# Kernel optimization log

Hardware: AMD Instinct MI355X
Metric: run time of the kernel (lower is better)

## Reference

```python
import jax, jax.numpy as jnp
import numpy as np


def setup_inputs() -> dict:
    key = jax.random.key(0)
    ks = jax.random.split(key, 8)
    b, s1, s2 = 16, 512, 40
    video_dim, text_dim, attn_dim = 1024, 300, 256
    return {
        "video": jax.random.normal(ks[0], (b, s1, video_dim), dtype=jnp.float32),
        "text": jax.random.normal(ks[1], (b, s2, text_dim), dtype=jnp.float32),
        "w1": jax.random.normal(ks[2], (video_dim, attn_dim), dtype=jnp.float32),
        "w2": jax.random.normal(ks[3], (text_dim, attn_dim), dtype=jnp.float32),
        "w3": jax.random.normal(ks[4], (attn_dim, 1), dtype=jnp.float32),
        "bias": jax.random.normal(ks[5], (attn_dim,), dtype=jnp.float32),
        "w4": jax.random.normal(ks[6], (4 * attn_dim, 500), dtype=jnp.float32),
        "b4": jax.random.normal(ks[7], (500,), dtype=jnp.float32),
    }


def reference(video, text, w1, w2, w3, bias, w4, b4):
    # video: (b, s1, d1), text: (b, s2, d2)
    e = jnp.einsum("bsd,da->bsa", video, w1)   # (b, s1, a) -- also 'hh' in original
    f = jnp.einsum("btd,da->bta", text, w2)    # (b, s2, a)
    # additive attention energies: tanh over (b, s1, s2, a) broadcast sum
    h = jnp.tanh(e[:, :, None, :] + f[:, None, :, :] + bias)  # (b, s1, s2, a)
    logits = jnp.squeeze(jnp.einsum("bsta,ao->bsto", h, w3), -1)  # (b, s1, s2)
    # original expands logits over attn_dim then softmaxes dim=2; identical to
    # softmax over s2 of the scalar scores, broadcast afterwards.
    attn = jax.nn.softmax(logits, axis=2)  # (b, s1, s2)
    text_attn = jnp.einsum("bst,bta->bsa", attn, f)  # (b, s1, a)
    cont = jnp.concatenate(
        [e, text_attn, e * text_attn, e - text_attn], axis=-1
    )  # (b, s1, 4a)
    return jnp.tanh(cont) @ w4 + b4  # (b, s1, 500)
```

## Files before the change

kernel.cpp:

```cpp
#include <hip/hip_runtime.h>
#include <hip/hip_bf16.h>
#include <cstdint>

typedef __attribute__((ext_vector_type(8))) short bf16x8;
typedef __attribute__((ext_vector_type(4))) short bf16x4;
typedef __attribute__((ext_vector_type(4))) float f32x4;

#define TANH_SCALE 2.8853900817779268f
#define TANH_UNSCALE 0.34657359027997264f

__device__ __forceinline__ short cvt_bf16(float f) {
  union { float f; uint32_t u; } x; x.f = f;
  uint32_t r = x.u + 0x7FFFu + ((x.u >> 16) & 1u);
  return (short)(r >> 16);
}
__device__ __forceinline__ float bf16_to_f(short s) {
  union { uint32_t u; float f; } x; x.u = ((uint32_t)(uint16_t)s) << 16;
  return x.f;
}

__device__ __forceinline__ float tanh_fast(float x) {
  float e = __builtin_amdgcn_exp2f(x * TANH_SCALE);
  return 1.0f - 2.0f * __builtin_amdgcn_rcpf(e + 1.0f);
}
__device__ __forceinline__ float sig_pre(float xs) {
  float e = __builtin_amdgcn_exp2f(xs);
  return __builtin_amdgcn_rcpf(e + 1.0f);
}

__device__ __forceinline__ void split8(float4 a, float4 b, bf16x8& h, bf16x8& l) {
  float fa[8] = {a.x, a.y, a.z, a.w, b.x, b.y, b.z, b.w};
  uint32_t uh[8], ul[8];
  #pragma unroll
  for (int j = 0; j < 8; j++) {
    union { float f; uint32_t u; } x; x.f = fa[j];
    uh[j] = x.u;
    union { uint32_t u; float f; } t; t.u = x.u & 0xffff0000u;
    union { float f; uint32_t u; } y; y.f = fa[j] - t.f;
    ul[j] = y.u;
  }
  union { uint32_t w[4]; bf16x8 v; } H, L;
  #pragma unroll
  for (int j = 0; j < 4; j++) {
    H.w[j] = __builtin_amdgcn_perm(uh[2 * j + 1], uh[2 * j], 0x07060302u);
    L.w[j] = __builtin_amdgcn_perm(ul[2 * j + 1], ul[2 * j], 0x07060302u);
  }
  h = H.v; l = L.v;
}

__global__ __launch_bounds__(256) void k_prep(const float* __restrict__ text,
                                              const float* __restrict__ w1,
                                              const float* __restrict__ w2,
                                              const float* __restrict__ w4,
                                              short* __restrict__ w1h,
                                              short* __restrict__ w1l,
                                              short* __restrict__ w4T,
                                              short* __restrict__ th,
                                              short* __restrict__ tl,
                                              short* __restrict__ w2h,
                                              short* __restrict__ w2l) {
  __shared__ float tile[32][33];
  int bid = blockIdx.x;
  if (bid < 256) {
    int idx = bid;
    int r0 = (idx & 31) * 32, c0 = (idx >> 5) * 32;
    int j = threadIdx.x & 31, i0 = threadIdx.x >> 5;
    #pragma unroll
    for (int i = i0; i < 32; i += 8) tile[i][j] = w1[(size_t)(r0 + i) * 256 + c0 + j];
    __syncthreads();
    #pragma unroll
    for (int i = i0; i < 32; i += 8) {
      float v = tile[j][i];
      short h = cvt_bf16(v);
      w1h[(size_t)(c0 + i) * 1024 + r0 + j] = h;
      w1l[(size_t)(c0 + i) * 1024 + r0 + j] = cvt_bf16(v - bf16_to_f(h));
    }
  } else if (bid < 768) {
    int idx = bid - 256;
    int r0 = (idx & 31) * 32, c0 = (idx >> 5) * 32;
    int j = threadIdx.x & 31, i0 = threadIdx.x >> 5;
    #pragma unroll
    for (int i = i0; i < 32; i += 8) {
      int c = c0 + j;
      tile[i][j] = (c < 500) ? w4[(size_t)(r0 + i) * 500 + c] : 0.f;
    }
    __syncthreads();
    #pragma unroll
    for (int i = i0; i < 32; i += 8)
      w4T[(size_t)(c0 + i) * 1024 + r0 + j] = cvt_bf16(tile[j][i]);
  } else if (bid < 928) {
    int idx = bid - 768;
    int row = idx * 4 + (threadIdx.x >> 6);
    int cl = threadIdx.x & 63;
    const float* trow = text + (size_t)row * 300;
    short* hrow = th + (size_t)row * 320;
    short* lrow = tl + (size_t)row * 320;
    #pragma unroll
    for (int c0 = 0; c0 < 320; c0 += 64) {
      int c = c0 + cl;
      float v = (c < 300) ? trow[c] : 0.f;
      short h = cvt_bf16(v);
      hrow[c] = h;
      lrow[c] = cvt_bf16(v - bf16_to_f(h));
    }
  } else {
    int idx = bid - 928;
    int rt = idx % 10, ct = idx / 10;
    int r0 = rt * 32, c0 = ct * 32;
    int j = threadIdx.x & 31, i0 = threadIdx.x >> 5;
    #pragma unroll
    for (int i = i0; i < 32; i += 8) {
      int r = r0 + i;
      tile[i][j] = (r < 300) ? w2[(size_t)r * 256 + c0 + j] : 0.f;
    }
    __syncthreads();
    #pragma unroll
    for (int i = i0; i < 32; i += 8) {
      float v = tile[j][i];
      short h = cvt_bf16(v);
      w2h[(size_t)(c0 + i) * 320 + r0 + j] = h;
      w2l[(size_t)(c0 + i) * 320 + r0 + j] = cvt_bf16(v - bf16_to_f(h));
    }
  }
}

__device__ __forceinline__ void load_lds16(void* lds, const void* g) {
  __builtin_amdgcn_global_load_lds(
      (const __attribute__((address_space(1))) void*)g,
      (__attribute__((address_space(3))) void*)lds, 16, 0, 0);
}

__global__ __launch_bounds__(256) void k_gemm_big(const float* __restrict__ video,
                                                  const short* __restrict__ w1h,
                                                  const short* __restrict__ w1l,
                                                  const short* __restrict__ th,
                                                  const short* __restrict__ tl,
                                                  const short* __restrict__ w2h,
                                                  const short* __restrict__ w2l,
                                                  float* __restrict__ eparts,
                                                  float* __restrict__ fbuf) {
  __shared__ __align__(16) char smem[65536];
  int bid = blockIdx.x;
  int tid = threadIdx.x, lane = tid & 63, wave = tid >> 6;
  int mrow = lane & 15, quad = lane >> 4;

  if (bid < 512) {
    short (*Ash)[64] = (short (*)[64])(smem);
    short (*Asl)[64] = (short (*)[64])(smem + 16384);
    int m0 = (bid & 63) * 128, n0 = ((bid >> 6) & 3) * 64;
    int z = bid >> 8;
    int kz0 = z * 512;
    int wm = wave * 32;
    int lrow = lane >> 3;
    int lsegsw = ((lane & 7) ^ lrow) * 8;

    f32x4 acc[2][4];
    #pragma unroll
    for (int i = 0; i < 2; i++)
      #pragma unroll
      for (int j = 0; j < 4; j++) acc[i][j] = (f32x4){0.f, 0.f, 0.f, 0.f};

    auto stageB = [&](int k0, int buf) {
      short* Bh = (short*)(smem + 32768 + buf * 8192);
      short* Bl = (short*)(smem + 49152 + buf * 8192);
      #pragma unroll
      for (int i = 0; i < 2; i++) {
        int c = wave * 2 + i;
        size_t go = (size_t)(n0 + c * 8 + lrow) * 1024 + k0 + lsegsw;
        load_lds16(Bh + (size_t)(c * 8) * 64, w1h + go);
        load_lds16(Bl + (size_t)(c * 8) * 64, w1l + go);
      }
    };
    auto loadA = [&](int k0, float4* va) {
      #pragma unroll
      for (int it = 0; it < 4; it++) {
        int idx = it * 256 + tid;
        const float* src = video + (size_t)(m0 + (idx >> 3)) * 1024 + k0 + (idx & 7) * 8;
        va[it * 2]     = *(const float4*)src;
        va[it * 2 + 1] = *(const float4*)(src + 4);
      }
    };

    float4 va[8];
    stageB(kz0, 0);
    loadA(kz0, va);

    for (int t = 0; t < 8; t++) {
      int k0 = kz0 + t * 64;
      int cur = t & 1;
      bf16x8 hi[4], lo[4];
      #pragma unroll
      for (int it = 0; it < 4; it++) split8(va[it * 2], va[it * 2 + 1], hi[it], lo[it]);
      __builtin_amdgcn_s_barrier();
      #pragma unroll
      for (int it = 0; it < 4; it++) {
        int idx = it * 256 + tid;
        int row = idx >> 3;
        int sw = ((idx & 7) ^ (row & 7)) * 8;
        *(bf16x8*)&Ash[row][sw] = hi[it];
        *(bf16x8*)&Asl[row][sw] = lo[it];
      }
      if (t + 1 < 8) {
        stageB(k0 + 64, cur ^ 1);
        loadA(k0 + 64, va);
        asm volatile("s_waitcnt vmcnt(12)" ::: "memory");
      } else {
        asm volatile("s_waitcnt vmcnt(0)" ::: "memory");
      }
      asm volatile("s_waitcnt lgkmcnt(0)" ::: "memory");
      __builtin_amdgcn_s_barrier();
      const short* Bh = (const short*)(smem + 32768 + cur * 8192);
      const short* Bl = (const short*)(smem + 49152 + cur * 8192);
      int rsw = mrow & 7;
      #pragma unroll
      for (int ks = 0; ks < 2; ks++) {
        int slot = ks * 4 + quad;
        int kko = ((slot ^ rsw) & 7) * 8;
        bf16x8 ah[2], al[2], bh[4], bl[4];
        #pragma unroll
        for (int i = 0; i < 2; i++) {
          ah[i] = *(const bf16x8*)&Ash[wm + i * 16 + mrow][kko];
          al[i] = *(const bf16x8*)&Asl[wm + i * 16 + mrow][kko];
        }
        #pragma unroll
        for (int j = 0; j < 4; j++) {
          bh[j] = *(const bf16x8*)&Bh[(size_t)(j * 16 + mrow) * 64 + kko];
          bl[j] = *(const bf16x8*)&Bl[(size_t)(j * 16 + mrow) * 64 + kko];
        }
        #pragma unroll
        for (int i = 0; i < 2; i++)
          #pragma unroll
          for (int j = 0; j < 4; j++) {
            acc[i][j] = __builtin_amdgcn_mfma_f32_16x16x32_bf16(ah[i], bh[j], acc[i][j], 0, 0, 0);
            acc[i][j] = __builtin_amdgcn_mfma_f32_16x16x32_bf16(ah[i], bl[j], acc[i][j], 0, 0, 0);
            acc[i][j] = __builtin_amdgcn_mfma_f32_16x16x32_bf16(al[i], bh[j], acc[i][j], 0, 0, 0);
          }
      }
    }
    float* C = eparts + (size_t)z * 8192 * 256;
    int rbase = quad * 4;
    #pragma unroll
    for (int i = 0; i < 2; i++)
      #pragma unroll
      for (int j = 0; j < 4; j++) {
        int col = n0 + j * 16 + mrow;
        #pragma unroll
        for (int r = 0; r < 4; r++) {
          int row = m0 + wm + i * 16 + rbase + r;
          C[(size_t)row * 256 + col] = acc[i][j][r];
        }
      }
  } else {
    short (*Ash)[72] = (short (*)[72])(smem);
    short (*Asl)[72] = (short (*)[72])(smem + 9216);
    short (*Bsh)[72] = (short (*)[72])(smem + 18432);
    short (*Bsl)[72] = (short (*)[72])(smem + 27648);
    int idx = bid - 512;
    int m0 = (idx % 10) * 64, n0 = (idx / 10) * 64;
    int wm = (wave & 1) * 32, wn = (wave >> 1) * 32;
    int srow = tid >> 3, sseg = (tid & 7) * 8;
    f32x4 acc[2][2];
    #pragma unroll
    for (int i = 0; i < 2; i++)
      #pragma unroll
      for (int j = 0; j < 2; j++) acc[i][j] = (f32x4){0.f, 0.f, 0.f, 0.f};

    for (int k0 = 0; k0 < 320; k0 += 64) {
      size_t aoff0 = (size_t)(m0 + srow) * 320 + k0 + sseg;
      size_t aoff1 = aoff0 + (size_t)32 * 320;
      size_t boff0 = (size_t)(n0 + srow) * 320 + k0 + sseg;
      size_t boff1 = boff0 + (size_t)32 * 320;
      bf16x8 a0h = *(const bf16x8*)(th + aoff0);
      bf16x8 a1h = *(const bf16x8*)(th + aoff1);
      bf16x8 a0l = *(const bf16x8*)(tl + aoff0);
      bf16x8 a1l = *(const bf16x8*)(tl + aoff1);
      bf16x8 b0h = *(const bf16x8*)(w2h + boff0);
      bf16x8 b1h = *(const bf16x8*)(w2h + boff1);
      bf16x8 b0l = *(const bf16x8*)(w2l + boff0);
      bf16x8 b1l = *(const bf16x8*)(w2l + boff1);
      __syncthreads();
      *(bf16x8*)&Ash[srow][sseg] = a0h;  *(bf16x8*)&Ash[srow + 32][sseg] = a1h;
      *(bf16x8*)&Asl[srow][sseg] = a0l;  *(bf16x8*)&Asl[srow + 32][sseg] = a1l;
      *(bf16x8*)&Bsh[srow][sseg] = b0h;  *(bf16x8*)&Bsh[srow + 32][sseg] = b1h;
      *(bf16x8*)&Bsl[srow][sseg] = b0l;  *(bf16x8*)&Bsl[srow + 32][sseg] = b1l;
      __syncthreads();
      #pragma unroll
      for (int ks = 0; ks < 2; ks++) {
        int kk = ks * 32 + quad * 8;
        bf16x8 ah[2], al[2], bh[2], bl[2];
        ah[0] = *(const bf16x8*)&Ash[wm + mrow][kk];
        ah[1] = *(const bf16x8*)&Ash[wm + 16 + mrow][kk];
        al[0] = *(const bf16x8*)&Asl[wm + mrow][kk];
        al[1] = *(const bf16x8*)&Asl[wm + 16 + mrow][kk];
        bh[0] = *(const bf16x8*)&Bsh[wn + mrow][kk];
        bh[1] = *(const bf16x8*)&Bsh[wn + 16 + mrow][kk];
        bl[0] = *(const bf16x8*)&Bsl[wn + mrow][kk];
        bl[1] = *(const bf16x8*)&Bsl[wn + 16 + mrow][kk];
        #pragma unroll
        for (int i = 0; i < 2; i++)
          #pragma unroll
          for (int j = 0; j < 2; j++) {
            acc[i][j] = __builtin_amdgcn_mfma_f32_16x16x32_bf16(ah[i], bh[j], acc[i][j], 0, 0, 0);
            acc[i][j] = __builtin_amdgcn_mfma_f32_16x16x32_bf16(ah[i], bl[j], acc[i][j], 0, 0, 0);
            acc[i][j] = __builtin_amdgcn_mfma_f32_16x16x32_bf16(al[i], bh[j], acc[i][j], 0, 0, 0);
          }
      }
    }
    int rbase = quad * 4;
    #pragma unroll
    for (int i = 0; i < 2; i++)
      #pragma unroll
      for (int j = 0; j < 2; j++) {
        int col = n0 + wn + j * 16 + mrow;
        #pragma unroll
        for (int r = 0; r < 4; r++) {
          int row = m0 + wm + i * 16 + rbase + r;
          fbuf[(size_t)row * 256 + col] = acc[i][j][r];
        }
      }
  }
}

__global__ __launch_bounds__(256) void k_gemm_f(const short* __restrict__ A,
                                                const short* __restrict__ BT,
                                                const float* __restrict__ bias,
                                                float* __restrict__ C,
                                                int K, int ldc, int nstore) {
  __shared__ __align__(16) short As[2][128][64];
  __shared__ __align__(16) short Bs[2][64][64];
  int m0 = blockIdx.x * 128, n0 = blockIdx.y * 64;
  int tid = threadIdx.x, lane = tid & 63, wave = tid >> 6;
  int wm = wave * 32;
  int mrow = lane & 15, quad = lane >> 4;
  int lrow = lane >> 3;
  int lsegsw = ((lane & 7) ^ lrow) * 8;

  f32x4 acc[2][4];
  #pragma unroll
  for (int i = 0; i < 2; i++)
    #pragma unroll
    for (int j = 0; j < 4; j++) acc[i][j] = (f32x4){0.f, 0.f, 0.f, 0.f};

  auto stage = [&](int k0, int buf) {
    #pragma unroll
    for (int i = 0; i < 4; i++) {
      int c = wave * 4 + i;
      load_lds16(&As[buf][c * 8][0], A + (size_t)(m0 + c * 8 + lrow) * K + k0 + lsegsw);
    }
    #pragma unroll
    for (int i = 0; i < 2; i++) {
      int c = wave * 2 + i;
      load_lds16(&Bs[buf][c * 8][0], BT + (size_t)(n0 + c * 8 + lrow) * K + k0 + lsegsw);
    }
  };

  int NT = K >> 6;
  stage(0, 0);
  int rsw = mrow & 7;
  for (int t = 0; t < NT; t++) {
    int cur = t & 1;
    if (t + 1 < NT) {
      stage((t + 1) << 6, cur ^ 1);
      asm volatile("s_waitcnt vmcnt(6)" ::: "memory");
    } else {
      asm volatile("s_waitcnt vmcnt(0)" ::: "memory");
    }
    __builtin_amdgcn_s_barrier();
    #pragma unroll
    for (int ks = 0; ks < 2; ks++) {
      int kko = (((ks * 4 + quad) ^ rsw) & 7) * 8;
      bf16x8 af[2], bf[4];
      #pragma unroll
      for (int i = 0; i < 2; i++) af[i] = *(const bf16x8*)&As[cur][wm + i * 16 + mrow][kko];
      #pragma unroll
      for (int j = 0; j < 4; j++) bf[j] = *(const bf16x8*)&Bs[cur][j * 16 + mrow][kko];
      #pragma unroll
      for (int i = 0; i < 2; i++)
        #pragma unroll
        for (int j = 0; j < 4; j++)
          acc[i][j] = __builtin_amdgcn_mfma_f32_16x16x32_bf16(af[i], bf[j], acc[i][j], 0, 0, 0);
    }
    __builtin_amdgcn_s_barrier();
  }
  int rbase = quad * 4;
  #pragma unroll
  for (int i = 0; i < 2; i++)
    #pragma unroll
    for (int j = 0; j < 4; j++) {
      int col = n0 + j * 16 + mrow;
      if (col < nstore) {
        float bv = bias[col];
        #pragma unroll
        for (int r = 0; r < 4; r++) {
          int row = m0 + wm + i * 16 + rbase + r;
          C[(size_t)row * ldc + col] = acc[i][j][r] + bv;
        }
      }
    }
}

__global__ __launch_bounds__(512) void k_middle(const float* __restrict__ e0p,
                                                const float* __restrict__ e1p,
                                                const float* __restrict__ fb,
                                                const float* __restrict__ w3,
                                                const float* __restrict__ bias,
                                                short* __restrict__ cont) {
  __shared__ __align__(16) float fbs[40 * 256];
  __shared__ float lg[16][40];
  __shared__ float attn[16][40];
  int tid = threadIdx.x, wave = tid >> 6, lane = tid & 63;
  int la = lane & 31, half = lane >> 5;
  int row0 = blockIdx.x * 16;
  int b = row0 >> 9;
  int lgrow = wave + (half ? 8 : 0);
  int myrow = row0 + lgrow;

  const float4* fsrc = (const float4*)(fb + (size_t)b * 40 * 256);
  const float4* bias4 = (const float4*)bias;
  for (int i = tid; i < 40 * 64; i += 512) {
    float4 v = fsrc[i];
    float4 bb = bias4[i & 63];
    v.x = (v.x + bb.x) * TANH_SCALE; v.y = (v.y + bb.y) * TANH_SCALE;
    v.z = (v.z + bb.z) * TANH_SCALE; v.w = (v.w + bb.w) * TANH_SCALE;
    ((float4*)fbs)[i] = v;
  }
  __syncthreads();

  int a0 = la * 8;
  size_t eoff = (size_t)myrow * 256 + a0;
  float4 p00 = *(const float4*)(e0p + eoff);
  float4 p01 = *(const float4*)(e0p + eoff + 4);
  float4 p10 = *(const float4*)(e1p + eoff);
  float4 p11 = *(const float4*)(e1p + eoff + 4);
  float4 e0, e1;
  e0.x = p00.x + p10.x; e0.y = p00.y + p10.y; e0.z = p00.z + p10.z; e0.w = p00.w + p10.w;
  e1.x = p01.x + p11.x; e1.y = p01.y + p11.y; e1.z = p01.z + p11.z; e1.w = p01.w + p11.w;
  float4 w30 = *(const float4*)(w3 + a0);
  float4 w31 = *(const float4*)(w3 + a0 + 4);
  w30.x *= -2.f; w30.y *= -2.f; w30.z *= -2.f; w30.w *= -2.f;
  w31.x *= -2.f; w31.y *= -2.f; w31.z *= -2.f; w31.w *= -2.f;
  float4 bv0 = *(const float4*)(bias + a0);
  float4 bv1 = *(const float4*)(bias + a0 + 4);
  float4 es0, es1;
  es0.x = e0.x * TANH_SCALE; es0.y = e0.y * TANH_SCALE;
  es0.z = e0.z * TANH_SCALE; es0.w = e0.w * TANH_SCALE;
  es1.x = e1.x * TANH_SCALE; es1.y = e1.y * TANH_SCALE;
  es1.z = e1.z * TANH_SCALE; es1.w = e1.w * TANH_SCALE;

  for (int tc = 0; tc < 40; tc += 4) {
    float p[4];
    #pragma unroll
    for (int u = 0; u < 4; u++) {
      const float* fr = &fbs[(tc + u) * 256 + a0];
      float4 f0 = *(const float4*)fr;
      float4 f1 = *(const float4*)(fr + 4);
      p[u] = sig_pre(es0.x + f0.x) * w30.x + sig_pre(es0.y + f0.y) * w30.y
           + sig_pre(es0.z + f0.z) * w30.z + sig_pre(es0.w + f0.w) * w30.w
           + sig_pre(es1.x + f1.x) * w31.x + sig_pre(es1.y + f1.y) * w31.y
           + sig_pre(es1.z + f1.z) * w31.z + sig_pre(es1.w + f1.w) * w31.w;
    }
    #pragma unroll
    for (int s = 16; s >= 1; s >>= 1) {
      #pragma unroll
      for (int u = 0; u < 4; u++) p[u] += __shfl_xor(p[u], s, 64);
    }
    if (la == 0) {
      #pragma unroll
      for (int u = 0; u < 4; u++) lg[lgrow][tc + u] = p[u];
    }
  }

  auto softmax_row = [&](int r) {
    float x = (lane < 40) ? lg[r][lane] : -3.0e38f;
    float m = x;
    #pragma unroll
    for (int s = 32; s >= 1; s >>= 1) m = fmaxf(m, __shfl_xor(m, s, 64));
    float ex = (lane < 40) ? __builtin_amdgcn_exp2f((x - m) * 1.4426950408889634f) : 0.f;
    float ssum = ex;
    #pragma unroll
    for (int s = 32; s >= 1; s >>= 1) ssum += __shfl_xor(ssum, s, 64);
    if (lane < 40) attn[r][lane] = ex * __builtin_amdgcn_rcpf(ssum);
  };
  softmax_row(wave);
  softmax_row(wave + 8);

  float ac[8] = {0.f,0.f,0.f,0.f,0.f,0.f,0.f,0.f};
  for (int t = 0; t < 40; t++) {
    float w = attn[lgrow][t];
    const float* fr = &fbs[t * 256 + a0];
    float4 f0 = *(const float4*)fr;
    float4 f1 = *(const float4*)(fr + 4);
    ac[0] += w * f0.x; ac[1] += w * f0.y; ac[2] += w * f0.z; ac[3] += w * f0.w;
    ac[4] += w * f1.x; ac[5] += w * f1.y; ac[6] += w * f1.z; ac[7] += w * f1.w;
  }
  float tx[8];
  tx[0] = ac[0] * TANH_UNSCALE - bv0.x; tx[1] = ac[1] * TANH_UNSCALE - bv0.y;
  tx[2] = ac[2] * TANH_UNSCALE - bv0.z; tx[3] = ac[3] * TANH_UNSCALE - bv0.w;
  tx[4] = ac[4] * TANH_UNSCALE - bv1.x; tx[5] = ac[5] * TANH_UNSCALE - bv1.y;
  tx[6] = ac[6] * TANH_UNSCALE - bv1.z; tx[7] = ac[7] * TANH_UNSCALE - bv1.w;
  float ev[8] = {e0.x, e0.y, e0.z, e0.w, e1.x, e1.y, e1.z, e1.w};

  short* crow = cont + (size_t)myrow * 1024 + a0;
  auto st8 = [&](int off, const float* v) {
    bf16x8 pk;
    #pragma unroll
    for (int i = 0; i < 8; i++) pk[i] = cvt_bf16(v[i]);
    *(bf16x8*)(crow + off) = pk;
  };
  float s0[8], s1[8], s2[8], s3[8];
  #pragma unroll
  for (int i = 0; i < 8; i++) {
    s0[i] = tanh_fast(ev[i]);
    s1[i] = tanh_fast(tx[i]);
    s2[i] = tanh_fast(ev[i] * tx[i]);
    s3[i] = tanh_fast(ev[i] - tx[i]);
  }
  st8(0, s0); st8(256, s1); st8(512, s2); st8(768, s3);
}

extern "C" void kernel_launch(void* const* d_in, const int* in_sizes, int n_in,
                              void* d_out, int out_size, void* d_ws, size_t ws_size,
                              hipStream_t stream) {
  const float* video = (const float*)d_in[0];
  const float* text  = (const float*)d_in[1];
  const float* w1    = (const float*)d_in[2];
  const float* w2    = (const float*)d_in[3];
  const float* w3    = (const float*)d_in[4];
  const float* bias  = (const float*)d_in[5];
  const float* w4    = (const float*)d_in[6];
  const float* b4    = (const float*)d_in[7];
  float* out = (float*)d_out;
  char* ws = (char*)d_ws;

  short* contbuf  = (short*)(ws);
  short* w1T_hi   = (short*)(ws + 16777216);
  short* w1T_lo   = (short*)(ws + 17301504);
  short* w4T      = (short*)(ws + 17825792);
  float* fbuf     = (float*)(ws + 18874368);
  float* eparts   = (float*)(ws + 19529728);
  float* epart1   = (float*)(ws + 19529728 + 8388608);
  short* text_hi  = (short*)(ws + 36306944);
  short* text_lo  = (short*)(ws + 36716544);
  short* w2T_hi   = (short*)(ws + 37126144);
  short* w2T_lo   = (short*)(ws + 37330944);

  k_prep<<<1008, 256, 0, stream>>>(text, w1, w2, w4,
                                   w1T_hi, w1T_lo, w4T,
                                   text_hi, text_lo, w2T_hi, w2T_lo);
  k_gemm_big<<<552, 256, 0, stream>>>(video, w1T_hi, w1T_lo,
                                      text_hi, text_lo, w2T_hi, w2T_lo,
                                      eparts, fbuf);
  k_middle<<<512, 512, 0, stream>>>(eparts, epart1, fbuf, w3, bias, contbuf);
  k_gemm_f<<<dim3(64, 8), 256, 0, stream>>>(contbuf, w4T, b4, out, 1024, 500, 500);
}
```

Measured before the change: 155.7 us.

## Load video A fragments directly into registers and move w4 transpose into k_middle

In the big GEMM, each wave now loads its own video rows straight into MFMA fragment layout and splits them into hi/lo bf16 in registers. This drops the A tile's trip through LDS and the extra lgkmcnt wait, and cuts shared memory from 64KB to 36KB so more blocks can be resident. The w4 transpose/convert work moves from k_prep into extra blocks of k_middle, shrinking the prep launch that sits on the critical path. The cost is less coalesced global loads for A (each lane reads 32-byte strided chunks) and a larger k_middle grid.

Result: slower. 163.0 us (+4.6%).

```diff
diff --git a/kernel.cpp b/kernel.cpp
--- a/kernel.cpp
+++ b/kernel.cpp
@@ -51,10 +51,8 @@
 __global__ __launch_bounds__(256) void k_prep(const float* __restrict__ text,
                                               const float* __restrict__ w1,
                                               const float* __restrict__ w2,
-                                              const float* __restrict__ w4,
                                               short* __restrict__ w1h,
                                               short* __restrict__ w1l,
-                                              short* __restrict__ w4T,
                                               short* __restrict__ th,
                                               short* __restrict__ tl,
                                               short* __restrict__ w2h,
@@ -75,21 +73,8 @@
       w1h[(size_t)(c0 + i) * 1024 + r0 + j] = h;
       w1l[(size_t)(c0 + i) * 1024 + r0 + j] = cvt_bf16(v - bf16_to_f(h));
     }
-  } else if (bid < 768) {
+  } else if (bid < 416) {
     int idx = bid - 256;
-    int r0 = (idx & 31) * 32, c0 = (idx >> 5) * 32;
-    int j = threadIdx.x & 31, i0 = threadIdx.x >> 5;
-    #pragma unroll
-    for (int i = i0; i < 32; i += 8) {
-      int c = c0 + j;
-      tile[i][j] = (c < 500) ? w4[(size_t)(r0 + i) * 500 + c] : 0.f;
-    }
-    __syncthreads();
-    #pragma unroll
-    for (int i = i0; i < 32; i += 8)
-      w4T[(size_t)(c0 + i) * 1024 + r0 + j] = cvt_bf16(tile[j][i]);
-  } else if (bid < 928) {
-    int idx = bid - 768;
     int row = idx * 4 + (threadIdx.x >> 6);
     int cl = threadIdx.x & 63;
     const float* trow = text + (size_t)row * 300;
@@ -104,7 +89,7 @@
       lrow[c] = cvt_bf16(v - bf16_to_f(h));
     }
   } else {
-    int idx = bid - 928;
+    int idx = bid - 416;
     int rt = idx % 10, ct = idx / 10;
     int r0 = rt * 32, c0 = ct * 32;
     int j = threadIdx.x & 31, i0 = threadIdx.x >> 5;
@@ -139,14 +124,12 @@
                                                   const short* __restrict__ w2l,
                                                   float* __restrict__ eparts,
                                                   float* __restrict__ fbuf) {
-  __shared__ __align__(16) char smem[65536];
+  __shared__ __align__(16) char smem[36864];
   int bid = blockIdx.x;
   int tid = threadIdx.x, lane = tid & 63, wave = tid >> 6;
   int mrow = lane & 15, quad = lane >> 4;
 
   if (bid < 512) {
-    short (*Ash)[64] = (short (*)[64])(smem);
-    short (*Asl)[64] = (short (*)[64])(smem + 16384);
     int m0 = (bid & 63) * 128, n0 = ((bid >> 6) & 3) * 64;
     int z = bid >> 8;
     int kz0 = z * 512;
@@ -161,8 +144,8 @@
       for (int j = 0; j < 4; j++) acc[i][j] = (f32x4){0.f, 0.f, 0.f, 0.f};
 
     auto stageB = [&](int k0, int buf) {
-      short* Bh = (short*)(smem + 32768 + buf * 8192);
-      short* Bl = (short*)(smem + 49152 + buf * 8192);
+      short* Bh = (short*)(smem + buf * 8192);
+      short* Bl = (short*)(smem + 16384 + buf * 8192);
       #pragma unroll
       for (int i = 0; i < 2; i++) {
         int c = wave * 2 + i;
@@ -171,57 +154,51 @@
         load_lds16(Bl + (size_t)(c * 8) * 64, w1l + go);
       }
     };
-    auto loadA = [&](int k0, float4* va) {
-      #pragma unroll
-      for (int it = 0; it < 4; it++) {
-        int idx = it * 256 + tid;
-        const float* src = video + (size_t)(m0 + (idx >> 3)) * 1024 + k0 + (idx & 7) * 8;
-        va[it * 2]     = *(const float4*)src;
-        va[it * 2 + 1] = *(const float4*)(src + 4);
+
+    const float* arow0 = video + (size_t)(m0 + wm + mrow) * 1024;
+    const float* arow1 = arow0 + (size_t)16 * 1024;
+    float4 va[8];
+    auto loadA = [&](int k0) {
+      #pragma unroll
+      for (int i = 0; i < 2; i++) {
+        const float* ar = i ? arow1 : arow0;
+        #pragma unroll
+        for (int ks = 0; ks < 2; ks++) {
+          const float* src = ar + k0 + ks * 32 + quad * 8;
+          va[(i * 2 + ks) * 2]     = *(const float4*)src;
+          va[(i * 2 + ks) * 2 + 1] = *(const float4*)(src + 4);
+        }
       }
     };
 
-    float4 va[8];
+    loadA(kz0);
     stageB(kz0, 0);
-    loadA(kz0, va);
-
+
+    int rsw = mrow & 7;
     for (int t = 0; t < 8; t++) {
       int k0 = kz0 + t * 64;
       int cur = t & 1;
-      bf16x8 hi[4], lo[4];
-      #pragma unroll
-      for (int it = 0; it < 4; it++) split8(va[it * 2], va[it * 2 + 1], hi[it], lo[it]);
+      bf16x8 ahp[2][2], alp[2][2];
+      #pragma unroll
+      for (int i = 0; i < 2; i++)
+        #pragma unroll
+        for (int ks = 0; ks < 2; ks++)
+          split8(va[(i * 2 + ks) * 2], va[(i * 2 + ks) * 2 + 1], ahp[i][ks], alp[i][ks]);
       __builtin_amdgcn_s_barrier();
-      #pragma unroll
-      for (int it = 0; it < 4; it++) {
-        int idx = it * 256 + tid;
-        int row = idx >> 3;
-        int sw = ((idx & 7) ^ (row & 7)) * 8;
-        *(bf16x8*)&Ash[row][sw] = hi[it];
-        *(bf16x8*)&Asl[row][sw] = lo[it];
-      }
       if (t + 1 < 8) {
+        loadA(k0 + 64);
         stageB(k0 + 64, cur ^ 1);
-        loadA(k0 + 64, va);
         asm volatile("s_waitcnt vmcnt(12)" ::: "memory");
       } else {
         asm volatile("s_waitcnt vmcnt(0)" ::: "memory");
       }
-      asm volatile("s_waitcnt lgkmcnt(0)" ::: "memory");
       __builtin_amdgcn_s_barrier();
-      const short* Bh = (const short*)(smem + 32768 + cur * 8192);
-      const short* Bl = (const short*)(smem + 49152 + cur * 8192);
-      int rsw = mrow & 7;
+      const short* Bh = (const short*)(smem + cur * 8192);
+      const short* Bl = (const short*)(smem + 16384 + cur * 8192);
       #pragma unroll
       for (int ks = 0; ks < 2; ks++) {
-        int slot = ks * 4 + quad;
-        int kko = ((slot ^ rsw) & 7) * 8;
-        bf16x8 ah[2], al[2], bh[4], bl[4];
-        #pragma unroll
-        for (int i = 0; i < 2; i++) {
-          ah[i] = *(const bf16x8*)&Ash[wm + i * 16 + mrow][kko];
-          al[i] = *(const bf16x8*)&Asl[wm + i * 16 + mrow][kko];
-        }
+        int kko = (((ks * 4 + quad) ^ rsw) & 7) * 8;
+        bf16x8 bh[4], bl[4];
         #pragma unroll
         for (int j = 0; j < 4; j++) {
           bh[j] = *(const bf16x8*)&Bh[(size_t)(j * 16 + mrow) * 64 + kko];
@@ -231,9 +208,9 @@
         for (int i = 0; i < 2; i++)
           #pragma unroll
           for (int j = 0; j < 4; j++) {
-            acc[i][j] = __builtin_amdgcn_mfma_f32_16x16x32_bf16(ah[i], bh[j], acc[i][j], 0, 0, 0);
-            acc[i][j] = __builtin_amdgcn_mfma_f32_16x16x32_bf16(ah[i], bl[j], acc[i][j], 0, 0, 0);
-            acc[i][j] = __builtin_amdgcn_mfma_f32_16x16x32_bf16(al[i], bh[j], acc[i][j], 0, 0, 0);
+            acc[i][j] = __builtin_amdgcn_mfma_f32_16x16x32_bf16(ahp[i][ks], bh[j], acc[i][j], 0, 0, 0);
+            acc[i][j] = __builtin_amdgcn_mfma_f32_16x16x32_bf16(ahp[i][ks], bl[j], acc[i][j], 0, 0, 0);
+            acc[i][j] = __builtin_amdgcn_mfma_f32_16x16x32_bf16(alp[i][ks], bh[j], acc[i][j], 0, 0, 0);
           }
       }
     }
@@ -404,11 +381,31 @@
                                                 const float* __restrict__ fb,
                                                 const float* __restrict__ w3,
                                                 const float* __restrict__ bias,
+                                                const float* __restrict__ w4,
+                                                short* __restrict__ w4T,
                                                 short* __restrict__ cont) {
   __shared__ __align__(16) float fbs[40 * 256];
   __shared__ float lg[16][40];
   __shared__ float attn[16][40];
   int tid = threadIdx.x, wave = tid >> 6, lane = tid & 63;
+
+  if (blockIdx.x >= 512) {
+    float* tile = fbs;
+    int idx = blockIdx.x - 512;
+    int r0 = (idx & 31) * 32, c0 = (idx >> 5) * 32;
+    int j = tid & 31, i0 = tid >> 5;
+    #pragma unroll
+    for (int i = i0; i < 32; i += 16) {
+      int c = c0 + j;
+      tile[i * 33 + j] = (c < 500) ? w4[(size_t)(r0 + i) * 500 + c] : 0.f;
+    }
+    __syncthreads();
+    #pragma unroll
+    for (int i = i0; i < 32; i += 16)
+      w4T[(size_t)(c0 + i) * 1024 + r0 + j] = cvt_bf16(tile[j * 33 + i]);
+    return;
+  }
+
   int la = lane & 31, half = lane >> 5;
   int row0 = blockIdx.x * 16;
   int b = row0 >> 9;
@@ -544,12 +541,12 @@
   short* w2T_hi   = (short*)(ws + 37126144);
   short* w2T_lo   = (short*)(ws + 37330944);
 
-  k_prep<<<1008, 256, 0, stream>>>(text, w1, w2, w4,
-                                   w1T_hi, w1T_lo, w4T,
-                                   text_hi, text_lo, w2T_hi, w2T_lo);
+  k_prep<<<496, 256, 0, stream>>>(text, w1, w2,
+                                  w1T_hi, w1T_lo,
+                                  text_hi, text_lo, w2T_hi, w2T_lo);
   k_gemm_big<<<552, 256, 0, stream>>>(video, w1T_hi, w1T_lo,
                                       text_hi, text_lo, w2T_hi, w2T_lo,
                                       eparts, fbuf);
-  k_middle<<<512, 512, 0, stream>>>(eparts, epart1, fbuf, w3, bias, contbuf);
+  k_middle<<<1024, 512, 0, stream>>>(eparts, epart1, fbuf, w3, bias, w4, w4T, contbuf);
   k_gemm_f<<<dim3(64, 8), 256, 0, stream>>>(contbuf, w4T, b4, out, 1024, 500, 500);
 }
```
